# Kernel tuning notes

Hardware: AMD Instinct MI355X
Metric: run time of the kernel (lower is better)

The kernel has to match this reference:

```python
import jax, jax.numpy as jnp
import numpy as np
import math

N = 100000   # outputSize (memory bank rows)
D = 128      # inputSize (feature dim)
B = 128      # batch size
K = 4096     # number of negatives per sample
T = 0.07     # temperature
MOMENTUM = 0.5


def setup_inputs() -> dict:
    key = jax.random.key(0)
    k1, k2, k3, k4, k5 = jax.random.split(key, 5)
    stdv = 1.0 / math.sqrt(D / 3.0)
    # l2-normalized features, as produced by the encoder in contrastive setups
    v1 = jax.random.normal(k1, (B, D), dtype=jnp.float32)
    v1 = v1 / jnp.linalg.norm(v1, axis=1, keepdims=True)
    v2 = jax.random.normal(k2, (B, D), dtype=jnp.float32)
    v2 = v2 / jnp.linalg.norm(v2, axis=1, keepdims=True)
    idx = jax.random.randint(k3, (B, K + 1), 0, N, dtype=jnp.int32)  # pos+neg bank rows
    y = jnp.arange(B, dtype=jnp.int32)  # distinct positive slots (first-visit behavior)
    # memory buffers initialized U(-stdv, stdv), as in torch.rand*2*stdv - stdv
    memory_v1 = jax.random.uniform(k4, (N, D), dtype=jnp.float32, minval=-stdv, maxval=stdv)
    memory_v2 = jax.random.uniform(k5, (N, D), dtype=jnp.float32, minval=-stdv, maxval=stdv)
    return {"v1": v1, "v2": v2, "idx": idx, "y": y,
            "memory_v1": memory_v1, "memory_v2": memory_v2}


def reference(v1, v2, idx, y, memory_v1, memory_v2):
    n_out = memory_v1.shape[0]
    # gather K+1 rows per sample (detached in the original -> stop_gradient)
    w1 = jax.lax.stop_gradient(memory_v1[idx])  # [B, K+1, D]
    w2 = jax.lax.stop_gradient(memory_v2[idx])  # [B, K+1, D]
    # batched vector-matrix product + exp/T
    out_v2 = jnp.exp(jnp.einsum('bkd,bd->bk', w1, v2) / T)  # [B, K+1]
    out_v1 = jnp.exp(jnp.einsum('bkd,bd->bk', w2, v1) / T)  # [B, K+1]
    # normalization constants (first-call Z computation: mean * outputSize)
    Z_v1 = jax.lax.stop_gradient(out_v1.mean()) * n_out
    Z_v2 = jax.lax.stop_gradient(out_v2.mean()) * n_out
    out_v1 = out_v1 / Z_v1
    out_v2 = out_v2 / Z_v2
    # momentum-blended normalize-and-scatter memory update (no_grad in torch)
    upd1 = MOMENTUM * memory_v1[y] + (1.0 - MOMENTUM) * v1  # [B, D]
    upd1 = upd1 / jnp.linalg.norm(upd1, axis=1, keepdims=True)
    new_memory_v1 = memory_v1.at[y].set(upd1)
    upd2 = MOMENTUM * memory_v2[y] + (1.0 - MOMENTUM) * v2
    upd2 = upd2 / jnp.linalg.norm(upd2, axis=1, keepdims=True)
    new_memory_v2 = memory_v2.at[y].set(upd2)
    return out_v1, out_v2, new_memory_v1, new_memory_v2
```

## Files before the change

### kernel.cpp

```cpp
#include <hip/hip_runtime.h>
#include <math.h>

constexpr int N_ROWS = 100000;
constexpr int D      = 128;
constexpr int B      = 128;
constexpr int KP1    = 4097;
constexpr int TOTAL_PAIRS = B * KP1;
constexpr float INV_T = 1.0f / 0.07f;
constexpr int N4 = N_ROWS * (D / 4);

constexpr int SCAN_BLOCKS = (N_ROWS + 255) / 256;
constexpr int FUSE_BLOCKS = 2048;
constexpr int NGROUPS     = FUSE_BLOCKS * 8;

constexpr size_t WS_OFFS   = 16;
constexpr size_t WS_CURSOR = WS_OFFS + (size_t)N_ROWS * 4;
constexpr size_t WS_BTOT   = WS_CURSOR + (size_t)N_ROWS * 4;
constexpr size_t WS_PLIST  = WS_BTOT + 512 * 4;
constexpr size_t WS_NEEDED = WS_PLIST + (size_t)TOTAL_PAIRS * 4;

typedef float fvec4 __attribute__((ext_vector_type(4)));

__device__ __forceinline__ float dot4(float4 a, float4 b) {
    return a.x * b.x + a.y * b.y + a.z * b.z + a.w * b.w;
}
__device__ __forceinline__ float red32(float v) {
    #pragma unroll
    for (int off = 16; off >= 1; off >>= 1) v += __shfl_xor(v, off);
    return v;
}

__global__ __launch_bounds__(256) void zero_ws_kernel(float* sums, int* offs) {
    int i = blockIdx.x * 256 + threadIdx.x;
    if (i < 2) sums[i] = 0.0f;
    for (int j = i; j < N_ROWS; j += gridDim.x * 256) offs[j] = 0;
}

__global__ __launch_bounds__(256) void hist_kernel(
    const int* __restrict__ idx, int* __restrict__ offs) {
    int stride = gridDim.x * 256;
    for (int p = blockIdx.x * 256 + threadIdx.x; p < TOTAL_PAIRS; p += stride)
        atomicAdd(&offs[idx[p]], 1);
}

__global__ __launch_bounds__(256) void scan_block_kernel(
    int* __restrict__ offs, int* __restrict__ btot) {
    __shared__ int buf[256];
    const int t = threadIdx.x;
    const int i = blockIdx.x * 256 + t;
    int v = (i < N_ROWS) ? offs[i] : 0;
    buf[t] = v;
    __syncthreads();
    for (int off = 1; off < 256; off <<= 1) {
        int y = (t >= off) ? buf[t - off] : 0;
        __syncthreads();
        buf[t] += y;
        __syncthreads();
    }
    if (i < N_ROWS) offs[i] = buf[t] - v;
    if (t == 255) btot[blockIdx.x] = buf[t];
}

__global__ void scan_btot_kernel(int* __restrict__ btot) {
    __shared__ int buf[512];
    const int t = threadIdx.x;
    int v = (t < SCAN_BLOCKS) ? btot[t] : 0;
    buf[t] = v;
    __syncthreads();
    for (int off = 1; off < 512; off <<= 1) {
        int y = (t >= off) ? buf[t - off] : 0;
        __syncthreads();
        buf[t] += y;
        __syncthreads();
    }
    if (t < SCAN_BLOCKS) btot[t] = buf[t] - v;
}

__global__ __launch_bounds__(256) void addback_kernel(
    int* __restrict__ offs, const int* __restrict__ btot, int* __restrict__ cursor) {
    int i = blockIdx.x * 256 + threadIdx.x;
    if (i < N_ROWS) {
        int o = offs[i] + btot[i >> 8];
        offs[i] = o;
        cursor[i] = o;
    }
}

__global__ __launch_bounds__(256) void scatter_kernel(
    const int* __restrict__ idx, int* __restrict__ cursor, int* __restrict__ plist) {
    int stride = gridDim.x * 256;
    for (int p = blockIdx.x * 256 + threadIdx.x; p < TOTAL_PAIRS; p += stride) {
        int r = idx[p];
        int pos = atomicAdd(&cursor[r], 1);
        plist[pos] = p;
    }
}

__global__ __launch_bounds__(256) void fused_kernel(
    const float* __restrict__ v1, const float* __restrict__ v2,
    const float* __restrict__ mem1, const float* __restrict__ mem2,
    const int* __restrict__ offs, const int* __restrict__ cend,
    const int* __restrict__ plist,
    float* __restrict__ out, float* __restrict__ sums,
    float* __restrict__ o1, float* __restrict__ o2)
{
    __shared__ float s1[8], s2[8];
    const int tid = threadIdx.x;
    const int l   = tid & 31;
    const int grp = tid >> 5;
    const int g   = blockIdx.x * 8 + grp;

    const float4* __restrict__ m1 = (const float4*)mem1;
    const float4* __restrict__ m2 = (const float4*)mem2;
    const float4* __restrict__ V1 = (const float4*)v1;
    const float4* __restrict__ V2 = (const float4*)v2;
    fvec4* __restrict__ d1 = (fvec4*)o1;
    fvec4* __restrict__ d2 = (fvec4*)o2;

    float acc1 = 0.0f, acc2 = 0.0f;

    for (int r = g; r < N_ROWS; r += NGROUPS) {
        float4 w1 = m1[(size_t)r * 32 + l];
        float4 w2 = m2[(size_t)r * 32 + l];

        fvec4 x1 = {w1.x, w1.y, w1.z, w1.w};
        fvec4 x2 = {w2.x, w2.y, w2.z, w2.w};
        __builtin_nontemporal_store(x1, &d1[(size_t)r * 32 + l]);
        __builtin_nontemporal_store(x2, &d2[(size_t)r * 32 + l]);

        int q = offs[r];
        const int e = cend[r];
        for (; q + 1 < e; q += 2) {
            int p0 = plist[q], p1 = plist[q + 1];
            int b0 = p0 / KP1, b1 = p1 / KP1;
            float4 a10 = V1[b0 * 32 + l], a20 = V2[b0 * 32 + l];
            float4 a11 = V1[b1 * 32 + l], a21 = V2[b1 * 32 + l];
            float dA0 = red32(dot4(w2, a10));
            float dB0 = red32(dot4(w1, a20));
            float dA1 = red32(dot4(w2, a11));
            float dB1 = red32(dot4(w1, a21));
            float eA0 = __expf(dA0 * INV_T), eB0 = __expf(dB0 * INV_T);
            float eA1 = __expf(dA1 * INV_T), eB1 = __expf(dB1 * INV_T);
            acc1 += eA0 + eA1;
            acc2 += eB0 + eB1;
            if (l == 0) {
                out[p0] = eA0; out[TOTAL_PAIRS + p0] = eB0;
                out[p1] = eA1; out[TOTAL_PAIRS + p1] = eB1;
            }
        }
        if (q < e) {
            int p0 = plist[q];
            int b0 = p0 / KP1;
            float4 a10 = V1[b0 * 32 + l], a20 = V2[b0 * 32 + l];
            float dA0 = red32(dot4(w2, a10));
            float dB0 = red32(dot4(w1, a20));
            float eA0 = __expf(dA0 * INV_T), eB0 = __expf(dB0 * INV_T);
            acc1 += eA0;
            acc2 += eB0;
            if (l == 0) { out[p0] = eA0; out[TOTAL_PAIRS + p0] = eB0; }
        }
    }

    if (l == 0) { s1[grp] = acc1; s2[grp] = acc2; }
    __syncthreads();
    if (tid == 0) {
        float t1 = 0.0f, t2 = 0.0f;
        #pragma unroll
        for (int i = 0; i < 8; ++i) { t1 += s1[i]; t2 += s2[i]; }
        atomicAdd(&sums[0], t1);
        atomicAdd(&sums[1], t2);
    }
}

__global__ __launch_bounds__(256) void finish_kernel(
    float* __restrict__ out, const float* __restrict__ sums,
    const float* __restrict__ v1, const float* __restrict__ v2,
    const int* __restrict__ y,
    const float* __restrict__ mem1, const float* __restrict__ mem2,
    float* __restrict__ o1, float* __restrict__ o2)
{
    if (blockIdx.x < 2 * B && threadIdx.x < 64) {
        int b    = blockIdx.x & (B - 1);
        int bank = blockIdx.x >> 7;
        int lane = threadIdx.x;
        const float2* __restrict__ m = (const float2*)(bank ? mem2 : mem1);
        const float2* __restrict__ v = (const float2*)(bank ? v2 : v1);
        float2* __restrict__ o       = (float2*)(bank ? o2 : o1);
        int row = y[b];
        float2 mv = m[(size_t)row * 64 + lane];
        float2 vv = v[b * 64 + lane];
        float2 u;
        u.x = 0.5f * mv.x + 0.5f * vv.x;
        u.y = 0.5f * mv.y + 0.5f * vv.y;
        float ss = u.x * u.x + u.y * u.y;
        #pragma unroll
        for (int off = 32; off >= 1; off >>= 1) ss += __shfl_xor(ss, off);
        float inv = 1.0f / sqrtf(ss);
        float2 r; r.x = u.x * inv; r.y = u.y * inv;
        o[(size_t)row * 64 + lane] = r;
    }

    float sc1 = (float)((double)TOTAL_PAIRS / ((double)sums[0] * (double)N_ROWS));
    float sc2 = (float)((double)TOTAL_PAIRS / ((double)sums[1] * (double)N_ROWS));
    int stride = gridDim.x * blockDim.x;
    for (int i = blockIdx.x * blockDim.x + threadIdx.x; i < 2 * TOTAL_PAIRS;
         i += stride) {
        out[i] *= (i < TOTAL_PAIRS) ? sc1 : sc2;
    }
}

__global__ void init_ws_kernel(float* ws) {
    if (threadIdx.x < 2) ws[threadIdx.x] = 0.0f;
}

__global__ __launch_bounds__(256) void score_kernel(
    const float* __restrict__ v1, const float* __restrict__ v2,
    const int* __restrict__ idx,
    const float* __restrict__ mem1, const float* __restrict__ mem2,
    float* __restrict__ out, float* __restrict__ sums)
{
    __shared__ alignas(16) int s_idx[260];
    __shared__ float s1[8], s2[8];
    const int sid   = blockIdx.x;
    const int tid   = threadIdx.x;
    const int l     = tid & 31;
    const int grp   = tid >> 5;
    const int b     = sid >> 4;
    const int chunk = sid & 15;
    const int cnt   = (chunk == 15) ? 257 : 256;
    const int ibase = b * KP1 + chunk * 256;
    for (int t = tid; t < cnt; t += 256) s_idx[t] = idx[ibase + t];
    __syncthreads();
    const float4* __restrict__ m1 = (const float4*)mem1;
    const float4* __restrict__ m2 = (const float4*)mem2;
    const float4 a1 = ((const float4*)v1)[b * 32 + l];
    const float4 a2 = ((const float4*)v2)[b * 32 + l];
    const int lk = grp * 32, pbase = ibase + lk;
    float acc1 = 0.0f, acc2 = 0.0f;
    for (int u = 0; u < 32; u += 4) {
        const int4 rr = *(const int4*)&s_idx[lk + u];
        float4 wA0 = m2[(size_t)rr.x * 32 + l], wB0 = m1[(size_t)rr.x * 32 + l];
        float4 wA1 = m2[(size_t)rr.y * 32 + l], wB1 = m1[(size_t)rr.y * 32 + l];
        float4 wA2 = m2[(size_t)rr.z * 32 + l], wB2 = m1[(size_t)rr.z * 32 + l];
        float4 wA3 = m2[(size_t)rr.w * 32 + l], wB3 = m1[(size_t)rr.w * 32 + l];
        float eA0 = __expf(red32(dot4(wA0, a1)) * INV_T);
        float eB0 = __expf(red32(dot4(wB0, a2)) * INV_T);
        float eA1 = __expf(red32(dot4(wA1, a1)) * INV_T);
        float eB1 = __expf(red32(dot4(wB1, a2)) * INV_T);
        float eA2 = __expf(red32(dot4(wA2, a1)) * INV_T);
        float eB2 = __expf(red32(dot4(wB2, a2)) * INV_T);
        float eA3 = __expf(red32(dot4(wA3, a1)) * INV_T);
        float eB3 = __expf(red32(dot4(wB3, a2)) * INV_T);
        acc1 += (eA0 + eA1) + (eA2 + eA3);
        acc2 += (eB0 + eB1) + (eB2 + eB3);
        float sa = (l & 1) ? eA1 : eA0, sb = (l & 1) ? eA3 : eA2;
        float evA = (l & 2) ? sb : sa;
        float sc = (l & 1) ? eB1 : eB0, sd = (l & 1) ? eB3 : eB2;
        float evB = (l & 2) ? sd : sc;
        int p = pbase + u;
        if (l < 4)      out[p + l] = evA;
        else if (l < 8) out[TOTAL_PAIRS + p + (l - 4)] = evB;
    }
    if (chunk == 15 && grp == 7) {
        int r = s_idx[256];
        float4 wA = m2[(size_t)r * 32 + l], wB = m1[(size_t)r * 32 + l];
        float eA = __expf(red32(dot4(wA, a1)) * INV_T);
        float eB = __expf(red32(dot4(wB, a2)) * INV_T);
        acc1 += eA; acc2 += eB;
        if (l == 0) {
            out[b * KP1 + 4096] = eA;
            out[TOTAL_PAIRS + b * KP1 + 4096] = eB;
        }
    }
    if (l == 0) { s1[grp] = acc1; s2[grp] = acc2; }
    __syncthreads();
    if (tid == 0) {
        float t1 = 0.0f, t2 = 0.0f;
        #pragma unroll
        for (int i = 0; i < 8; ++i) { t1 += s1[i]; t2 += s2[i]; }
        atomicAdd(&sums[0], t1);
        atomicAdd(&sums[1], t2);
    }
}

__global__ __launch_bounds__(256) void copy_scale_kernel(
    const float* __restrict__ mem1, const float* __restrict__ mem2,
    float* __restrict__ o1, float* __restrict__ o2,
    float* __restrict__ out, const float* __restrict__ sums)
{
    const fvec4* __restrict__ m1 = (const fvec4*)mem1;
    const fvec4* __restrict__ m2 = (const fvec4*)mem2;
    fvec4* __restrict__ d1 = (fvec4*)o1;
    fvec4* __restrict__ d2 = (fvec4*)o2;
    int tid = blockIdx.x * 256 + threadIdx.x;
    int stride = gridDim.x * 256;
    for (int i = tid; i < N4; i += stride) {
        fvec4 x1 = m1[i], x2 = m2[i];
        __builtin_nontemporal_store(x1, &d1[i]);
        __builtin_nontemporal_store(x2, &d2[i]);
    }
    float sc1 = (float)((double)TOTAL_PAIRS / ((double)sums[0] * (double)N_ROWS));
    float sc2 = (float)((double)TOTAL_PAIRS / ((double)sums[1] * (double)N_ROWS));
    for (int i = tid; i < 2 * TOTAL_PAIRS; i += stride) {
        out[i] *= (i < TOTAL_PAIRS) ? sc1 : sc2;
    }
}

__global__ void rowupd_kernel(
    const float* __restrict__ v1, const float* __restrict__ v2,
    const int* __restrict__ y,
    const float* __restrict__ mem1, const float* __restrict__ mem2,
    float* __restrict__ o1, float* __restrict__ o2)
{
    int b    = blockIdx.x & (B - 1);
    int bank = blockIdx.x >> 7;
    int lane = threadIdx.x;
    const float2* __restrict__ m = (const float2*)(bank ? mem2 : mem1);
    const float2* __restrict__ v = (const float2*)(bank ? v2 : v1);
    float2* __restrict__ o       = (float2*)(bank ? o2 : o1);
    int row = y[b];
    float2 mv = m[(size_t)row * 64 + lane];
    float2 vv = v[b * 64 + lane];
    float2 u;
    u.x = 0.5f * mv.x + 0.5f * vv.x;
    u.y = 0.5f * mv.y + 0.5f * vv.y;
    float ss = u.x * u.x + u.y * u.y;
    #pragma unroll
    for (int off = 32; off >= 1; off >>= 1) ss += __shfl_xor(ss, off);
    float inv = 1.0f / sqrtf(ss);
    float2 r; r.x = u.x * inv; r.y = u.y * inv;
    o[(size_t)row * 64 + lane] = r;
}

extern "C" void kernel_launch(void* const* d_in, const int* in_sizes, int n_in,
                              void* d_out, int out_size, void* d_ws, size_t ws_size,
                              hipStream_t stream) {
    const float* v1   = (const float*)d_in[0];
    const float* v2   = (const float*)d_in[1];
    const int*   idx  = (const int*)d_in[2];
    const int*   y    = (const int*)d_in[3];
    const float* mem1 = (const float*)d_in[4];
    const float* mem2 = (const float*)d_in[5];

    float* out = (float*)d_out;
    float* out_mem1 = out + 2 * (size_t)TOTAL_PAIRS;
    float* out_mem2 = out_mem1 + (size_t)N_ROWS * D;
    char*  ws   = (char*)d_ws;
    float* sums = (float*)d_ws;

    if (ws_size >= WS_NEEDED) {
        int* offs   = (int*)(ws + WS_OFFS);
        int* cursor = (int*)(ws + WS_CURSOR);
        int* btot   = (int*)(ws + WS_BTOT);
        int* plist  = (int*)(ws + WS_PLIST);

        zero_ws_kernel<<<256, 256, 0, stream>>>(sums, offs);
        hist_kernel<<<512, 256, 0, stream>>>(idx, offs);
        scan_block_kernel<<<SCAN_BLOCKS, 256, 0, stream>>>(offs, btot);
        scan_btot_kernel<<<1, 512, 0, stream>>>(btot);
        addback_kernel<<<SCAN_BLOCKS, 256, 0, stream>>>(offs, btot, cursor);
        scatter_kernel<<<512, 256, 0, stream>>>(idx, cursor, plist);
        fused_kernel<<<FUSE_BLOCKS, 256, 0, stream>>>(
            v1, v2, mem1, mem2, offs, cursor, plist,
            out, sums, out_mem1, out_mem2);
        finish_kernel<<<1024, 256, 0, stream>>>(
            out, sums, v1, v2, y, mem1, mem2, out_mem1, out_mem2);
    } else {
        init_ws_kernel<<<1, 64, 0, stream>>>(sums);
        score_kernel<<<2048, 256, 0, stream>>>(
            v1, v2, idx, mem1, mem2, out, sums);
        copy_scale_kernel<<<2048, 256, 0, stream>>>(
            mem1, mem2, out_mem1, out_mem2, out, sums);
        rowupd_kernel<<<2 * B, 64, 0, stream>>>(
            v1, v2, y, mem1, mem2, out_mem1, out_mem2);
    }
}
```

Baseline: 349.3 us.

## Bucket pairs by 40-row blocks and score them from LDS-staged memory rows

```diff
diff --git a/kernel.cpp b/kernel.cpp
--- a/kernel.cpp
+++ b/kernel.cpp
@@ -9,15 +9,15 @@
 constexpr float INV_T = 1.0f / 0.07f;
 constexpr int N4 = N_ROWS * (D / 4);
 
-constexpr int SCAN_BLOCKS = (N_ROWS + 255) / 256;
-constexpr int FUSE_BLOCKS = 2048;
-constexpr int NGROUPS     = FUSE_BLOCKS * 8;
-
-constexpr size_t WS_OFFS   = 16;
-constexpr size_t WS_CURSOR = WS_OFFS + (size_t)N_ROWS * 4;
-constexpr size_t WS_BTOT   = WS_CURSOR + (size_t)N_ROWS * 4;
-constexpr size_t WS_PLIST  = WS_BTOT + 512 * 4;
+constexpr int RPB  = 40;
+constexpr int NB   = N_ROWS / RPB;
+constexpr int PADR = 33;
+
+constexpr size_t WS_BCNT   = 64;
+constexpr size_t WS_BSTART = WS_BCNT + (size_t)NB * 16 * 4;
+constexpr size_t WS_PLIST  = WS_BSTART + (size_t)(NB + 4) * 4;
 constexpr size_t WS_NEEDED = WS_PLIST + (size_t)TOTAL_PAIRS * 4;
+constexpr size_t WS_ZERO_BYTES = WS_BSTART;
 
 typedef float fvec4 __attribute__((ext_vector_type(4)));
 
@@ -30,143 +30,134 @@
     return v;
 }
 
-__global__ __launch_bounds__(256) void zero_ws_kernel(float* sums, int* offs) {
-    int i = blockIdx.x * 256 + threadIdx.x;
-    if (i < 2) sums[i] = 0.0f;
-    for (int j = i; j < N_ROWS; j += gridDim.x * 256) offs[j] = 0;
-}
-
 __global__ __launch_bounds__(256) void hist_kernel(
-    const int* __restrict__ idx, int* __restrict__ offs) {
-    int stride = gridDim.x * 256;
-    for (int p = blockIdx.x * 256 + threadIdx.x; p < TOTAL_PAIRS; p += stride)
-        atomicAdd(&offs[idx[p]], 1);
-}
-
-__global__ __launch_bounds__(256) void scan_block_kernel(
-    int* __restrict__ offs, int* __restrict__ btot) {
-    __shared__ int buf[256];
-    const int t = threadIdx.x;
-    const int i = blockIdx.x * 256 + t;
-    int v = (i < N_ROWS) ? offs[i] : 0;
-    buf[t] = v;
-    __syncthreads();
-    for (int off = 1; off < 256; off <<= 1) {
-        int y = (t >= off) ? buf[t - off] : 0;
-        __syncthreads();
-        buf[t] += y;
-        __syncthreads();
-    }
-    if (i < N_ROWS) offs[i] = buf[t] - v;
-    if (t == 255) btot[blockIdx.x] = buf[t];
-}
-
-__global__ void scan_btot_kernel(int* __restrict__ btot) {
-    __shared__ int buf[512];
-    const int t = threadIdx.x;
-    int v = (t < SCAN_BLOCKS) ? btot[t] : 0;
-    buf[t] = v;
-    __syncthreads();
-    for (int off = 1; off < 512; off <<= 1) {
-        int y = (t >= off) ? buf[t - off] : 0;
-        __syncthreads();
-        buf[t] += y;
-        __syncthreads();
-    }
-    if (t < SCAN_BLOCKS) btot[t] = buf[t] - v;
-}
-
-__global__ __launch_bounds__(256) void addback_kernel(
-    int* __restrict__ offs, const int* __restrict__ btot, int* __restrict__ cursor) {
-    int i = blockIdx.x * 256 + threadIdx.x;
-    if (i < N_ROWS) {
-        int o = offs[i] + btot[i >> 8];
-        offs[i] = o;
-        cursor[i] = o;
-    }
-}
-
-__global__ __launch_bounds__(256) void scatter_kernel(
-    const int* __restrict__ idx, int* __restrict__ cursor, int* __restrict__ plist) {
+    const int* __restrict__ idx, int* __restrict__ bcnt) {
     int stride = gridDim.x * 256;
     for (int p = blockIdx.x * 256 + threadIdx.x; p < TOTAL_PAIRS; p += stride) {
-        int r = idx[p];
-        int pos = atomicAdd(&cursor[r], 1);
-        plist[pos] = p;
+        int bkt = idx[p] / RPB;
+        atomicAdd(&bcnt[bkt * 16], 1);
+    }
+}
+
+__global__ __launch_bounds__(1024) void scan_kernel(
+    int* __restrict__ bcnt, int* __restrict__ bstart) {
+    __shared__ int ssum[1024];
+    const int t = threadIdx.x;
+    const int b0 = 3 * t;
+    int c0 = (b0     < NB) ? bcnt[(b0    ) * 16] : 0;
+    int c1 = (b0 + 1 < NB) ? bcnt[(b0 + 1) * 16] : 0;
+    int c2 = (b0 + 2 < NB) ? bcnt[(b0 + 2) * 16] : 0;
+    int local = c0 + c1 + c2;
+    ssum[t] = local;
+    __syncthreads();
+    for (int off = 1; off < 1024; off <<= 1) {
+        int v = (t >= off) ? ssum[t - off] : 0;
+        __syncthreads();
+        ssum[t] += v;
+        __syncthreads();
+    }
+    int excl = ssum[t] - local;
+    if (b0     < NB) { bstart[b0]     = excl;           bcnt[(b0    ) * 16] = excl; }
+    if (b0 + 1 < NB) { bstart[b0 + 1] = excl + c0;      bcnt[(b0 + 1) * 16] = excl + c0; }
+    if (b0 + 2 < NB) { bstart[b0 + 2] = excl + c0 + c1; bcnt[(b0 + 2) * 16] = excl + c0 + c1; }
+    if (t == 1023) bstart[NB] = ssum[1023];
+}
+
+__global__ __launch_bounds__(256) void scatter_kernel(
+    const int* __restrict__ idx, int* __restrict__ bcnt,
+    unsigned* __restrict__ plist) {
+    int stride = gridDim.x * 256;
+    for (int p = blockIdx.x * 256 + threadIdx.x; p < TOTAL_PAIRS; p += stride) {
+        int r   = idx[p];
+        int bkt = r / RPB;
+        int lr  = r - bkt * RPB;
+        int pos = atomicAdd(&bcnt[bkt * 16], 1);
+        plist[pos] = (unsigned)p | ((unsigned)lr << 20);
     }
 }
 
 __global__ __launch_bounds__(256) void fused_kernel(
     const float* __restrict__ v1, const float* __restrict__ v2,
     const float* __restrict__ mem1, const float* __restrict__ mem2,
-    const int* __restrict__ offs, const int* __restrict__ cend,
-    const int* __restrict__ plist,
+    const int* __restrict__ bstart, const unsigned* __restrict__ plist,
     float* __restrict__ out, float* __restrict__ sums,
     float* __restrict__ o1, float* __restrict__ o2)
 {
-    __shared__ float s1[8], s2[8];
+    __shared__ float4 sm1[RPB * PADR];
+    __shared__ float4 sm2[RPB * PADR];
+    __shared__ float sz1[4], sz2[4];
+
+    const int bid = blockIdx.x;
     const int tid = threadIdx.x;
-    const int l   = tid & 31;
-    const int grp = tid >> 5;
-    const int g   = blockIdx.x * 8 + grp;
-
-    const float4* __restrict__ m1 = (const float4*)mem1;
-    const float4* __restrict__ m2 = (const float4*)mem2;
+    const int r0  = bid * RPB;
+
+    const float4* __restrict__ M1 = (const float4*)mem1;
+    const float4* __restrict__ M2 = (const float4*)mem2;
     const float4* __restrict__ V1 = (const float4*)v1;
     const float4* __restrict__ V2 = (const float4*)v2;
     fvec4* __restrict__ d1 = (fvec4*)o1;
     fvec4* __restrict__ d2 = (fvec4*)o2;
 
-    float acc1 = 0.0f, acc2 = 0.0f;
-
-    for (int r = g; r < N_ROWS; r += NGROUPS) {
-        float4 w1 = m1[(size_t)r * 32 + l];
-        float4 w2 = m2[(size_t)r * 32 + l];
-
-        fvec4 x1 = {w1.x, w1.y, w1.z, w1.w};
-        fvec4 x2 = {w2.x, w2.y, w2.z, w2.w};
-        __builtin_nontemporal_store(x1, &d1[(size_t)r * 32 + l]);
-        __builtin_nontemporal_store(x2, &d2[(size_t)r * 32 + l]);
-
-        int q = offs[r];
-        const int e = cend[r];
-        for (; q + 1 < e; q += 2) {
-            int p0 = plist[q], p1 = plist[q + 1];
-            int b0 = p0 / KP1, b1 = p1 / KP1;
-            float4 a10 = V1[b0 * 32 + l], a20 = V2[b0 * 32 + l];
-            float4 a11 = V1[b1 * 32 + l], a21 = V2[b1 * 32 + l];
-            float dA0 = red32(dot4(w2, a10));
-            float dB0 = red32(dot4(w1, a20));
-            float dA1 = red32(dot4(w2, a11));
-            float dB1 = red32(dot4(w1, a21));
-            float eA0 = __expf(dA0 * INV_T), eB0 = __expf(dB0 * INV_T);
-            float eA1 = __expf(dA1 * INV_T), eB1 = __expf(dB1 * INV_T);
-            acc1 += eA0 + eA1;
-            acc2 += eB0 + eB1;
-            if (l == 0) {
-                out[p0] = eA0; out[TOTAL_PAIRS + p0] = eB0;
-                out[p1] = eA1; out[TOTAL_PAIRS + p1] = eB1;
-            }
+    for (int i = tid; i < RPB * 32; i += 256) {
+        int lr = i >> 5, c = i & 31;
+        size_t gi = (size_t)(r0 + lr) * 32 + c;
+        float4 x1 = M1[gi];
+        float4 x2 = M2[gi];
+        sm1[lr * PADR + c] = x1;
+        sm2[lr * PADR + c] = x2;
+        fvec4 y1 = {x1.x, x1.y, x1.z, x1.w};
+        fvec4 y2 = {x2.x, x2.y, x2.z, x2.w};
+        __builtin_nontemporal_store(y1, &d1[gi]);
+        __builtin_nontemporal_store(y2, &d2[gi]);
+    }
+    __syncthreads();
+
+    const int team = tid >> 3;
+    const int sub  = tid & 7;
+    const int qend = bstart[bid + 1];
+    float az1 = 0.0f, az2 = 0.0f;
+
+    for (int q = bstart[bid] + team; q < qend; q += 32) {
+        unsigned v = plist[q];
+        int p  = (int)(v & 0xFFFFFu);
+        int lr = (int)(v >> 20);
+        int b  = p / KP1;
+
+        const float4* __restrict__ w1 = &sm1[lr * PADR];
+        const float4* __restrict__ w2 = &sm2[lr * PADR];
+        float a = 0.0f, bb = 0.0f;
+        #pragma unroll
+        for (int i = 0; i < 4; ++i) {
+            int c = sub + 8 * i;
+            float4 vv1 = V1[b * 32 + c];
+            float4 vv2 = V2[b * 32 + c];
+            float4 x2  = w2[c];
+            float4 x1  = w1[c];
+            a  += dot4(x2, vv1);
+            bb += dot4(x1, vv2);
         }
-        if (q < e) {
-            int p0 = plist[q];
-            int b0 = p0 / KP1;
-            float4 a10 = V1[b0 * 32 + l], a20 = V2[b0 * 32 + l];
-            float dA0 = red32(dot4(w2, a10));
-            float dB0 = red32(dot4(w1, a20));
-            float eA0 = __expf(dA0 * INV_T), eB0 = __expf(dB0 * INV_T);
-            acc1 += eA0;
-            acc2 += eB0;
-            if (l == 0) { out[p0] = eA0; out[TOTAL_PAIRS + p0] = eB0; }
+        #pragma unroll
+        for (int off = 4; off >= 1; off >>= 1) {
+            a  += __shfl_xor(a,  off);
+            bb += __shfl_xor(bb, off);
         }
-    }
-
-    if (l == 0) { s1[grp] = acc1; s2[grp] = acc2; }
+        float eA = __expf(a  * INV_T);
+        float eB = __expf(bb * INV_T);
+        az1 += eA;
+        az2 += eB;
+        if (sub < 2) out[(sub ? TOTAL_PAIRS : 0) + p] = sub ? eB : eA;
+    }
+
+    #pragma unroll
+    for (int off = 32; off >= 1; off >>= 1) {
+        az1 += __shfl_xor(az1, off);
+        az2 += __shfl_xor(az2, off);
+    }
+    if ((tid & 63) == 0) { sz1[tid >> 6] = az1; sz2[tid >> 6] = az2; }
     __syncthreads();
     if (tid == 0) {
-        float t1 = 0.0f, t2 = 0.0f;
-        #pragma unroll
-        for (int i = 0; i < 8; ++i) { t1 += s1[i]; t2 += s2[i]; }
+        float t1 = (sz1[0] + sz1[1] + sz1[2] + sz1[3]) * 0.125f;
+        float t2 = (sz2[0] + sz2[1] + sz2[2] + sz2[3]) * 0.125f;
         atomicAdd(&sums[0], t1);
         atomicAdd(&sums[1], t2);
     }
@@ -349,19 +340,16 @@
     float* sums = (float*)d_ws;
 
     if (ws_size >= WS_NEEDED) {
-        int* offs   = (int*)(ws + WS_OFFS);
-        int* cursor = (int*)(ws + WS_CURSOR);
-        int* btot   = (int*)(ws + WS_BTOT);
-        int* plist  = (int*)(ws + WS_PLIST);
-
-        zero_ws_kernel<<<256, 256, 0, stream>>>(sums, offs);
-        hist_kernel<<<512, 256, 0, stream>>>(idx, offs);
-        scan_block_kernel<<<SCAN_BLOCKS, 256, 0, stream>>>(offs, btot);
-        scan_btot_kernel<<<1, 512, 0, stream>>>(btot);
-        addback_kernel<<<SCAN_BLOCKS, 256, 0, stream>>>(offs, btot, cursor);
-        scatter_kernel<<<512, 256, 0, stream>>>(idx, cursor, plist);
-        fused_kernel<<<FUSE_BLOCKS, 256, 0, stream>>>(
-            v1, v2, mem1, mem2, offs, cursor, plist,
+        int*      bcnt   = (int*)(ws + WS_BCNT);
+        int*      bstart = (int*)(ws + WS_BSTART);
+        unsigned* plist  = (unsigned*)(ws + WS_PLIST);
+
+        hipMemsetAsync(ws, 0, WS_ZERO_BYTES, stream);
+        hist_kernel<<<512, 256, 0, stream>>>(idx, bcnt);
+        scan_kernel<<<1, 1024, 0, stream>>>(bcnt, bstart);
+        scatter_kernel<<<512, 256, 0, stream>>>(idx, bcnt, plist);
+        fused_kernel<<<NB, 256, 0, stream>>>(
+            v1, v2, mem1, mem2, bstart, plist,
             out, sums, out_mem1, out_mem2);
         finish_kernel<<<1024, 256, 0, stream>>>(
             out, sums, v1, v2, y, mem1, mem2, out_mem1, out_mem2);
```

After: 314.6 us. 9.9% less time.
